# Kernel optimization log

Measured on AMD Instinct MI355X. Metric: run time of the kernel, lower is better.

The kernel has to match this reference:

```python
import jax, jax.numpy as jnp
import numpy as np

H = 32            # tsm_horizon
UNIT = H * 16     # block stride (512)
W = UNIT + H      # window size incl. h-step lookahead (544)
EPS = 1e-12

def setup_inputs() -> dict:
    key = jax.random.key(0)
    features = jax.random.normal(key, (8, 64, 8192), dtype=jnp.float32)
    return {"features": features}

def reference(features):
    # features: [B, C, L]  (post-TCN feature map); L divisible by UNIT
    B, C, L = features.shape
    nblocks = L // UNIT
    # pad L with H zeros so every block window has size W; corrcoef between two
    # time steps depends only on those two columns, so padded columns never
    # contaminate valid entries (they are masked out below).
    padded = jnp.pad(features, ((0, 0), (0, 0), (0, H)))
    starts = jnp.arange(nblocks) * UNIT                     # [n]
    idx = starts[:, None] + jnp.arange(W)[None, :]          # [n, W]
    windows = padded[:, :, idx]                             # [B, C, n, W]
    # corrcoef over channels: variables = time steps, observations = channels
    Xc = windows - windows.mean(axis=1, keepdims=True)      # center over C
    num = jnp.einsum('bcnw,bcnv->bnwv', Xc, Xc)             # [B, n, W, W]
    norm = jnp.sqrt(jnp.einsum('bcnw,bcnw->bnw', Xc, Xc))   # [B, n, W]
    corr = num / jnp.maximum(norm[..., :, None] * norm[..., None, :], EPS)
    # extract superdiagonal band: tsm[t, k] = corr[t, t+1+k], t<UNIT, k<H
    t = jnp.arange(UNIT)
    cols = t[:, None] + 1 + jnp.arange(H)[None, :]          # [UNIT, H]
    band = corr[:, :, t[:, None], cols]                     # [B, n, UNIT, H]
    # entries whose global column index falls beyond L are zero (torch pads 0)
    gcol = starts[:, None, None] + cols[None, :, :]         # [n, UNIT, H]
    band = jnp.where(gcol[None] < L, band, jnp.zeros((), band.dtype))
    tsm = band.reshape(B, L, H).transpose(0, 2, 1)          # [B, H, L]
    return tsm
```

## Files before the change

kernel.cpp:

```cpp
#include <hip/hip_runtime.h>
#include <math.h>

#define CC    64
#define LL    8192
#define HH    32
#define UNITL 512
#define TC    128
#define WC    160
#define XSTR  72
#define BSTR  132
#define EPSF  1e-12f

typedef __attribute__((ext_vector_type(8))) short bf16x8;
typedef __attribute__((ext_vector_type(4))) float f32x4;
typedef __attribute__((ext_vector_type(4))) unsigned int u32x4;

union U {
    unsigned int xs[32][WC];
    struct {
        float band[HH][BSTR];
        float ms[WC];
        float ns[WC];
    } s;
};

__device__ __forceinline__ unsigned rne_bf16(unsigned ub) {
    return (ub + 0x7FFFu + ((ub >> 16) & 1u)) >> 16;
}
__device__ __forceinline__ float bf16_to_f(unsigned short h) {
    return __uint_as_float(((unsigned)h) << 16);
}

__global__ __launch_bounds__(512, 4)
void tsm_kernel(const float* __restrict__ feat, float* __restrict__ out) {
    __shared__ U u;
    __shared__ short xhi[WC * XSTR];
    __shared__ short xlo[WC * XSTR];

    const int tid  = threadIdx.x;
    const int lane = tid & 63;
    const int wv   = tid >> 6;
    const int blk  = blockIdx.x;
    const int q4   = blk & 3;
    const int n    = (blk >> 2) & 15;
    const int b    = blk >> 6;
    const int col0 = n * UNITL + q4 * TC;

    const float* fb = feat + (size_t)b * CC * LL;

    for (int chunk = 0; chunk < 2; ++chunk) {
        #pragma unroll
        for (int it = 0; it < 3; ++it) {
            int tau = it * 512 + tid;
            if (tau < 32 * (WC / 4)) {
                int c  = tau / (WC / 4);
                int qq = tau - c * (WC / 4);
                int l  = col0 + 4 * qq;
                f32x4 v = {0.f, 0.f, 0.f, 0.f};
                if (l < LL)
                    v = *reinterpret_cast<const f32x4*>(fb + (size_t)(chunk * 32 + c) * LL + l);
                u32x4 pk;
                #pragma unroll
                for (int e = 0; e < 4; ++e) {
                    unsigned ub = __float_as_uint(v[e]);
                    unsigned hr = rne_bf16(ub);
                    float lo = v[e] - __uint_as_float(hr << 16);
                    unsigned lr = rne_bf16(__float_as_uint(lo));
                    pk[e] = (hr << 16) | (lr & 0xFFFFu);
                }
                *reinterpret_cast<u32x4*>(&u.xs[c][4 * qq]) = pk;
            }
        }
        __syncthreads();
        #pragma unroll
        for (int it = 0; it < 2; ++it) {
            int tau = it * 512 + tid;
            if (tau < 4 * WC) {
                int c8 = tau / WC;
                int w  = tau - c8 * WC;
                bf16x8 Hv, Lv;
                #pragma unroll
                for (int j = 0; j < 8; ++j) {
                    unsigned p = u.xs[c8 * 8 + j][w];
                    Hv[j] = (short)(p >> 16);
                    Lv[j] = (short)(p & 0xFFFFu);
                }
                int base = w * XSTR + chunk * 32 + c8 * 8;
                *reinterpret_cast<bf16x8*>(&xhi[base]) = Hv;
                *reinterpret_cast<bf16x8*>(&xlo[base]) = Lv;
            }
        }
        __syncthreads();
    }

    if (tid < WC) {
        float s = 0.f, ss = 0.f;
        #pragma unroll
        for (int k = 0; k < 8; ++k) {
            bf16x8 Hv = *reinterpret_cast<const bf16x8*>(&xhi[tid * XSTR + 8 * k]);
            bf16x8 Lv = *reinterpret_cast<const bf16x8*>(&xlo[tid * XSTR + 8 * k]);
            #pragma unroll
            for (int j = 0; j < 8; ++j) {
                float x = bf16_to_f((unsigned short)Hv[j]) + bf16_to_f((unsigned short)Lv[j]);
                s += x; ss += x * x;
            }
        }
        float m = s * (1.0f / CC);
        u.s.ms[tid] = m;
        u.s.ns[tid] = sqrtf(fmaxf(ss - (float)CC * m * m, 0.f));
    }
    {
        const int r16 = lane & 15;
        const int g   = lane >> 4;
        bf16x8 fh[3][2], fl[3][2];
        #pragma unroll
        for (int bb = 0; bb < 3; ++bb) {
            int row  = 16 * (wv + bb) + r16;
            int base = row * XSTR;
            #pragma unroll
            for (int kk = 0; kk < 2; ++kk) {
                int off = base + (g + 4 * kk) * 8;
                fh[bb][kk] = *reinterpret_cast<const bf16x8*>(&xhi[off]);
                fl[bb][kk] = *reinterpret_cast<const bf16x8*>(&xlo[off]);
            }
        }
        #pragma unroll
        for (int dj = 0; dj < 3; ++dj) {
            f32x4 acc = {0.f, 0.f, 0.f, 0.f};
            acc = __builtin_amdgcn_mfma_f32_16x16x32_bf16(fh[0][0], fh[dj][0], acc, 0, 0, 0);
            acc = __builtin_amdgcn_mfma_f32_16x16x32_bf16(fh[0][1], fh[dj][1], acc, 0, 0, 0);
            acc = __builtin_amdgcn_mfma_f32_16x16x32_bf16(fh[0][0], fl[dj][0], acc, 0, 0, 0);
            acc = __builtin_amdgcn_mfma_f32_16x16x32_bf16(fh[0][1], fl[dj][1], acc, 0, 0, 0);
            acc = __builtin_amdgcn_mfma_f32_16x16x32_bf16(fl[0][0], fh[dj][0], acc, 0, 0, 0);
            acc = __builtin_amdgcn_mfma_f32_16x16x32_bf16(fl[0][1], fh[dj][1], acc, 0, 0, 0);
            #pragma unroll
            for (int r = 0; r < 4; ++r) {
                int t  = 16 * wv + 4 * g + r;
                int tp = 16 * (wv + dj) + r16;
                int h  = tp - t - 1;
                if ((unsigned)h < 32u) u.s.band[h][t] = acc[r];
            }
        }
    }
    __syncthreads();

    {
        const int h  = tid >> 4;
        const int cb = tid & 15;
        float* ob = out + ((size_t)b * HH + h) * LL + col0;
        #pragma unroll
        for (int k = 0; k < 2; ++k) {
            int t0 = 4 * (cb + 16 * k);
            f32x4 v = *reinterpret_cast<const f32x4*>(&u.s.band[h][t0]);
            f32x4 res;
            #pragma unroll
            for (int e = 0; e < 4; ++e) {
                int t  = t0 + e;
                int tp = t + 1 + h;
                float num  = v[e] - (float)CC * u.s.ms[t] * u.s.ms[tp];
                float den  = fmaxf(u.s.ns[t] * u.s.ns[tp], EPSF);
                float corr = num * __builtin_amdgcn_rcpf(den);
                if (col0 + tp >= LL) corr = 0.f;
                res[e] = corr;
            }
            *reinterpret_cast<f32x4*>(ob + t0) = res;
        }
    }
}

extern "C" void kernel_launch(void* const* d_in, const int* in_sizes, int n_in,
                              void* d_out, int out_size, void* d_ws, size_t ws_size,
                              hipStream_t stream) {
    const float* feat = (const float*)d_in[0];
    float* out = (float*)d_out;
    tsm_kernel<<<dim3(512), dim3(512), 0, stream>>>(feat, out);
}
```

Baseline: 13.53 us.

## Halve tile width, stage fp32 once and split to bf16 hi/lo in registers

Shrinks the per-block time tile from 128 to 64 columns and launches 1024 blocks of 256 threads instead of 512 blocks of 512. All 64 channels are loaded into shared memory as fp32 in a single pass. The bf16 hi/lo split now happens directly in registers while building MFMA fragments, which removes the two-chunk packed staging and the transpose buffers. This cuts shared-memory passes and barriers, but the halo overhead grows (96-wide window for 64 outputs) and the per-element bf16 conversion work is repeated across the waves that share rows.

```diff
diff --git a/kernel.cpp b/kernel.cpp
--- a/kernel.cpp
+++ b/kernel.cpp
@@ -5,18 +5,18 @@
 #define LL    8192
 #define HH    32
 #define UNITL 512
-#define TC    128
-#define WC    160
-#define XSTR  72
-#define BSTR  132
+#define TC    64
+#define WC    96
+#define STR   98
+#define BSTR  68
 #define EPSF  1e-12f
 
 typedef __attribute__((ext_vector_type(8))) short bf16x8;
 typedef __attribute__((ext_vector_type(4))) float f32x4;
-typedef __attribute__((ext_vector_type(4))) unsigned int u32x4;
+typedef __attribute__((ext_vector_type(2))) float f32x2;
 
 union U {
-    unsigned int xs[32][WC];
+    float xs[CC][STR];
     struct {
         float band[HH][BSTR];
         float ms[WC];
@@ -27,130 +27,93 @@
 __device__ __forceinline__ unsigned rne_bf16(unsigned ub) {
     return (ub + 0x7FFFu + ((ub >> 16) & 1u)) >> 16;
 }
-__device__ __forceinline__ float bf16_to_f(unsigned short h) {
-    return __uint_as_float(((unsigned)h) << 16);
-}
 
-__global__ __launch_bounds__(512, 4)
+__global__ __launch_bounds__(256, 4)
 void tsm_kernel(const float* __restrict__ feat, float* __restrict__ out) {
     __shared__ U u;
-    __shared__ short xhi[WC * XSTR];
-    __shared__ short xlo[WC * XSTR];
 
     const int tid  = threadIdx.x;
     const int lane = tid & 63;
     const int wv   = tid >> 6;
     const int blk  = blockIdx.x;
-    const int q4   = blk & 3;
-    const int n    = (blk >> 2) & 15;
-    const int b    = blk >> 6;
-    const int col0 = n * UNITL + q4 * TC;
+    const int q8   = blk & 7;
+    const int n    = (blk >> 3) & 15;
+    const int b    = blk >> 7;
+    const int col0 = n * UNITL + q8 * TC;
 
     const float* fb = feat + (size_t)b * CC * LL;
 
-    for (int chunk = 0; chunk < 2; ++chunk) {
+    #pragma unroll
+    for (int it = 0; it < 6; ++it) {
+        int tau = it * 256 + tid;
+        int c   = tau / 24;
+        int q   = tau - c * 24;
+        int l   = col0 + 4 * q;
+        f32x4 v = {0.f, 0.f, 0.f, 0.f};
+        if (l < LL) v = *reinterpret_cast<const f32x4*>(fb + (size_t)c * LL + l);
+        *reinterpret_cast<f32x2*>(&u.xs[c][4 * q])     = (f32x2){v[0], v[1]};
+        *reinterpret_cast<f32x2*>(&u.xs[c][4 * q + 2]) = (f32x2){v[2], v[3]};
+    }
+    __syncthreads();
+
+    const int r16 = lane & 15;
+    const int g   = lane >> 4;
+    bf16x8 fh[3][2], fl[3][2];
+    #pragma unroll
+    for (int bb = 0; bb < 3; ++bb) {
+        int row = 16 * (wv + bb) + r16;
         #pragma unroll
-        for (int it = 0; it < 3; ++it) {
-            int tau = it * 512 + tid;
-            if (tau < 32 * (WC / 4)) {
-                int c  = tau / (WC / 4);
-                int qq = tau - c * (WC / 4);
-                int l  = col0 + 4 * qq;
-                f32x4 v = {0.f, 0.f, 0.f, 0.f};
-                if (l < LL)
-                    v = *reinterpret_cast<const f32x4*>(fb + (size_t)(chunk * 32 + c) * LL + l);
-                u32x4 pk;
-                #pragma unroll
-                for (int e = 0; e < 4; ++e) {
-                    unsigned ub = __float_as_uint(v[e]);
-                    unsigned hr = rne_bf16(ub);
-                    float lo = v[e] - __uint_as_float(hr << 16);
-                    unsigned lr = rne_bf16(__float_as_uint(lo));
-                    pk[e] = (hr << 16) | (lr & 0xFFFFu);
-                }
-                *reinterpret_cast<u32x4*>(&u.xs[c][4 * qq]) = pk;
+        for (int kk = 0; kk < 2; ++kk) {
+            int cb = 8 * g + 32 * kk;
+            #pragma unroll
+            for (int j = 0; j < 8; ++j) {
+                float x = u.xs[cb + j][row];
+                unsigned ub = __float_as_uint(x);
+                unsigned hr = rne_bf16(ub);
+                float lo = x - __uint_as_float(hr << 16);
+                unsigned lr = rne_bf16(__float_as_uint(lo));
+                fh[bb][kk][j] = (short)hr;
+                fl[bb][kk][j] = (short)lr;
             }
         }
-        __syncthreads();
-        #pragma unroll
-        for (int it = 0; it < 2; ++it) {
-            int tau = it * 512 + tid;
-            if (tau < 4 * WC) {
-                int c8 = tau / WC;
-                int w  = tau - c8 * WC;
-                bf16x8 Hv, Lv;
-                #pragma unroll
-                for (int j = 0; j < 8; ++j) {
-                    unsigned p = u.xs[c8 * 8 + j][w];
-                    Hv[j] = (short)(p >> 16);
-                    Lv[j] = (short)(p & 0xFFFFu);
-                }
-                int base = w * XSTR + chunk * 32 + c8 * 8;
-                *reinterpret_cast<bf16x8*>(&xhi[base]) = Hv;
-                *reinterpret_cast<bf16x8*>(&xlo[base]) = Lv;
-            }
-        }
-        __syncthreads();
     }
-
+    float m = 0.f, nr = 0.f;
     if (tid < WC) {
         float s = 0.f, ss = 0.f;
         #pragma unroll
-        for (int k = 0; k < 8; ++k) {
-            bf16x8 Hv = *reinterpret_cast<const bf16x8*>(&xhi[tid * XSTR + 8 * k]);
-            bf16x8 Lv = *reinterpret_cast<const bf16x8*>(&xlo[tid * XSTR + 8 * k]);
-            #pragma unroll
-            for (int j = 0; j < 8; ++j) {
-                float x = bf16_to_f((unsigned short)Hv[j]) + bf16_to_f((unsigned short)Lv[j]);
-                s += x; ss += x * x;
-            }
-        }
-        float m = s * (1.0f / CC);
-        u.s.ms[tid] = m;
-        u.s.ns[tid] = sqrtf(fmaxf(ss - (float)CC * m * m, 0.f));
+        for (int c = 0; c < CC; ++c) { float x = u.xs[c][tid]; s += x; ss += x * x; }
+        m  = s * (1.0f / CC);
+        nr = sqrtf(fmaxf(ss - (float)CC * m * m, 0.f));
     }
-    {
-        const int r16 = lane & 15;
-        const int g   = lane >> 4;
-        bf16x8 fh[3][2], fl[3][2];
+    __syncthreads();
+
+    if (tid < WC) { u.s.ms[tid] = m; u.s.ns[tid] = nr; }
+    #pragma unroll
+    for (int dj = 0; dj < 3; ++dj) {
+        f32x4 acc = {0.f, 0.f, 0.f, 0.f};
+        acc = __builtin_amdgcn_mfma_f32_16x16x32_bf16(fh[0][0], fh[dj][0], acc, 0, 0, 0);
+        acc = __builtin_amdgcn_mfma_f32_16x16x32_bf16(fh[0][1], fh[dj][1], acc, 0, 0, 0);
+        acc = __builtin_amdgcn_mfma_f32_16x16x32_bf16(fh[0][0], fl[dj][0], acc, 0, 0, 0);
+        acc = __builtin_amdgcn_mfma_f32_16x16x32_bf16(fh[0][1], fl[dj][1], acc, 0, 0, 0);
+        acc = __builtin_amdgcn_mfma_f32_16x16x32_bf16(fl[0][0], fh[dj][0], acc, 0, 0, 0);
+        acc = __builtin_amdgcn_mfma_f32_16x16x32_bf16(fl[0][1], fh[dj][1], acc, 0, 0, 0);
         #pragma unroll
-        for (int bb = 0; bb < 3; ++bb) {
-            int row  = 16 * (wv + bb) + r16;
-            int base = row * XSTR;
-            #pragma unroll
-            for (int kk = 0; kk < 2; ++kk) {
-                int off = base + (g + 4 * kk) * 8;
-                fh[bb][kk] = *reinterpret_cast<const bf16x8*>(&xhi[off]);
-                fl[bb][kk] = *reinterpret_cast<const bf16x8*>(&xlo[off]);
-            }
-        }
-        #pragma unroll
-        for (int dj = 0; dj < 3; ++dj) {
-            f32x4 acc = {0.f, 0.f, 0.f, 0.f};
-            acc = __builtin_amdgcn_mfma_f32_16x16x32_bf16(fh[0][0], fh[dj][0], acc, 0, 0, 0);
-            acc = __builtin_amdgcn_mfma_f32_16x16x32_bf16(fh[0][1], fh[dj][1], acc, 0, 0, 0);
-            acc = __builtin_amdgcn_mfma_f32_16x16x32_bf16(fh[0][0], fl[dj][0], acc, 0, 0, 0);
-            acc = __builtin_amdgcn_mfma_f32_16x16x32_bf16(fh[0][1], fl[dj][1], acc, 0, 0, 0);
-            acc = __builtin_amdgcn_mfma_f32_16x16x32_bf16(fl[0][0], fh[dj][0], acc, 0, 0, 0);
-            acc = __builtin_amdgcn_mfma_f32_16x16x32_bf16(fl[0][1], fh[dj][1], acc, 0, 0, 0);
-            #pragma unroll
-            for (int r = 0; r < 4; ++r) {
-                int t  = 16 * wv + 4 * g + r;
-                int tp = 16 * (wv + dj) + r16;
-                int h  = tp - t - 1;
-                if ((unsigned)h < 32u) u.s.band[h][t] = acc[r];
-            }
+        for (int r = 0; r < 4; ++r) {
+            int t  = 16 * wv + 4 * g + r;
+            int tp = 16 * (wv + dj) + r16;
+            int h  = tp - t - 1;
+            if ((unsigned)h < 32u) u.s.band[h][t] = acc[r];
         }
     }
     __syncthreads();
 
     {
-        const int h  = tid >> 4;
-        const int cb = tid & 15;
+        const int h   = tid >> 3;
+        const int cb8 = tid & 7;
         float* ob = out + ((size_t)b * HH + h) * LL + col0;
         #pragma unroll
         for (int k = 0; k < 2; ++k) {
-            int t0 = 4 * (cb + 16 * k);
+            int t0 = 4 * (cb8 + 8 * k);
             f32x4 v = *reinterpret_cast<const f32x4*>(&u.s.band[h][t0]);
             f32x4 res;
             #pragma unroll
@@ -173,5 +136,5 @@
                               hipStream_t stream) {
     const float* feat = (const float*)d_in[0];
     float* out = (float*)d_out;
-    tsm_kernel<<<dim3(512), dim3(512), 0, stream>>>(feat, out);
+    tsm_kernel<<<dim3(1024), dim3(256), 0, stream>>>(feat, out);
 }
```

New measurement: 13.78 us. No clear change (+1.9%).
